# Kernel tuning notes

Measured on AMD Instinct MI355X. Metric: run time of the kernel, lower is better.

The kernel has to match this reference:

```python
import jax, jax.numpy as jnp
import numpy as np

B, N, DIM, K, H, R = 128, 196, 384, 16, 6, 4  # batch, tokens, channels, bases, heads, adapter ratio


def setup_inputs() -> dict:
    key = jax.random.key(0)
    ks = jax.random.split(key, 4)
    d_r = DIM // R
    return {
        "x": jax.random.normal(ks[0], (B, N, DIM), jnp.float32),
        "W1": jax.random.normal(ks[1], (DIM, d_r), jnp.float32) * 0.02,
        "b1": jnp.zeros((d_r,), jnp.float32),
        "W2": jax.random.normal(ks[2], (d_r, K * H), jnp.float32) * 0.02,
        "b2": jnp.zeros((K * H,), jnp.float32),
        "weight_bank": jax.random.normal(ks[3], (K, N, N), jnp.float32) * 0.02,
    }


def reference(x, W1, b1, W2, b2, weight_bank):
    Bsz, n, C = x.shape
    hdim = C // H
    # adapter MLP: Linear -> GELU(exact/erf, torch default) -> Linear
    hid = jax.nn.gelu(x @ W1 + b1, approximate=False)
    mix = (hid @ W2 + b2).reshape(Bsz, n, K, H)
    # mode='softmax': normalize mixing policy over the k bases
    mix = jax.nn.softmax(mix, axis=2)
    # dynamic per-sample token-mixing matrix [B, n, n, H]
    weight = jnp.einsum('bnkh,knm->bnmh', mix, weight_bank)
    # mix tokens: contract over source token index n
    xh = x.reshape(Bsz, n, H, hdim)
    out = jnp.einsum('bnhc,bnmh->bmhc', xh, weight).reshape(Bsz, n, C)
    return out
```

## Files before the change

kernel.cpp:

```cpp
#include <hip/hip_runtime.h>
#include <math.h>

#define BB  128
#define NN  196
#define CDIM 384
#define KK  16
#define HH  6
#define DR  96
#define HD  64
#define MP  208
#define NCHUNK 7
#define PLANE 6656

typedef __attribute__((ext_vector_type(8))) short bf16x8;
typedef __attribute__((ext_vector_type(4))) float f32x4;

__device__ __forceinline__ unsigned short f2bf(float f) {
    unsigned u = __float_as_uint(f);
    u += 0x7FFFu + ((u >> 16) & 1u);
    return (unsigned short)(u >> 16);
}
__device__ __forceinline__ unsigned pk2bf(float lo, float hi) {
    return (unsigned)f2bf(lo) | ((unsigned)f2bf(hi) << 16);
}

union AFrag { unsigned u[4]; bf16x8 f; };

__global__ __launch_bounds__(256) void prep_kernel(
    const float* __restrict__ W1, const float* __restrict__ W2,
    const float* __restrict__ wb,
    unsigned short* __restrict__ W1T, unsigned short* __restrict__ W2T,
    unsigned short* __restrict__ wbT)
{
    const int bid = blockIdx.x;
    const int t   = threadIdx.x;
    if (bid < DR) {
        const int c = bid;
        for (int k = t; k < CDIM; k += 256)
            W1T[(size_t)c * CDIM + k] = f2bf(W1[(size_t)k * DR + c]);
        if (t < DR)
            W2T[(size_t)c * DR + t] = f2bf(W2[(size_t)t * DR + c]);
    } else {
        const int n = bid - DR;
        const int m = t;
        if (m < MP) {
            unsigned o[8] = {0u, 0u, 0u, 0u, 0u, 0u, 0u, 0u};
            if (n < NN && m < NN) {
                #pragma unroll
                for (int j = 0; j < 8; ++j) {
                    const float a = wb[((size_t)(2 * j)     * NN + n) * NN + m];
                    const float c = wb[((size_t)(2 * j + 1) * NN + n) * NN + m];
                    o[j] = pk2bf(a, c);
                }
            }
            unsigned* dst = (unsigned*)(wbT + ((size_t)n * MP + m) * KK);
            *(uint4*)dst       = make_uint4(o[0], o[1], o[2], o[3]);
            *(uint4*)(dst + 4) = make_uint4(o[4], o[5], o[6], o[7]);
        }
    }
}

__global__ __launch_bounds__(256, 3) void mixa_kernel(
    const float* __restrict__ x,  const unsigned short* __restrict__ W1T,
    const float* __restrict__ b1, const unsigned short* __restrict__ W2T,
    const float* __restrict__ b2, const unsigned short* __restrict__ wbT,
    unsigned short* __restrict__ A)
{
    __shared__ unsigned short hidb[32][104];
    __shared__ unsigned short msc[32][96];

    const int t    = threadIdx.x;
    const int w    = t >> 6;
    const int wm   = w & 1;
    const int wc   = w >> 1;
    const int lane = t & 63;
    const int l15  = lane & 15;
    const int lq   = lane >> 4;
    const int b    = blockIdx.x & 127;
    const int nc   = blockIdx.x >> 7;
    const int n0   = nc * 32;

    f32x4 acc[3];
    #pragma unroll
    for (int ct = 0; ct < 3; ++ct) {
        const float bj = b1[wc * 48 + ct * 16 + l15];
        acc[ct] = (f32x4){bj, bj, bj, bj};
    }
    const int nrow = n0 + wm * 16 + l15;
    const bool rv  = (nrow < NN);
    const float* xrow = x + ((size_t)b * NN + nrow) * CDIM;
    float4 u = make_float4(0.f, 0.f, 0.f, 0.f);
    float4 v = make_float4(0.f, 0.f, 0.f, 0.f);
    if (rv) {
        u = *(const float4*)(xrow + 8 * lq);
        v = *(const float4*)(xrow + 8 * lq + 4);
    }
    for (int kc = 0; kc < CDIM; kc += 32) {
        float4 un = make_float4(0.f, 0.f, 0.f, 0.f);
        float4 vn = make_float4(0.f, 0.f, 0.f, 0.f);
        if (rv && kc + 32 < CDIM) {
            un = *(const float4*)(xrow + kc + 32 + 8 * lq);
            vn = *(const float4*)(xrow + kc + 32 + 8 * lq + 4);
        }
        __builtin_amdgcn_sched_barrier(0);
        AFrag af;
        af.u[0] = pk2bf(u.x, u.y); af.u[1] = pk2bf(u.z, u.w);
        af.u[2] = pk2bf(v.x, v.y); af.u[3] = pk2bf(v.z, v.w);
        #pragma unroll
        for (int ct = 0; ct < 3; ++ct) {
            const bf16x8 bf = *(const bf16x8*)(W1T + (size_t)(wc * 48 + ct * 16 + l15) * CDIM + kc + 8 * lq);
            acc[ct] = __builtin_amdgcn_mfma_f32_16x16x32_bf16(af.f, bf, acc[ct], 0, 0, 0);
        }
        __builtin_amdgcn_sched_barrier(0);
        u = un; v = vn;
    }
    #pragma unroll
    for (int ct = 0; ct < 3; ++ct)
        #pragma unroll
        for (int r = 0; r < 4; ++r) {
            const float vv = acc[ct][r];
            hidb[wm * 16 + lq * 4 + r][wc * 48 + ct * 16 + l15] =
                f2bf(0.5f * vv * (1.0f + erff(vv * 0.70710678118654752f)));
        }
    __syncthreads();

    f32x4 acc2[3];
    #pragma unroll
    for (int ct = 0; ct < 3; ++ct) {
        const float bj = b2[wc * 48 + ct * 16 + l15];
        acc2[ct] = (f32x4){bj, bj, bj, bj};
    }
    #pragma unroll
    for (int kc = 0; kc < DR; kc += 32) {
        const bf16x8 af = *(const bf16x8*)&hidb[wm * 16 + l15][kc + 8 * lq];
        #pragma unroll
        for (int ct = 0; ct < 3; ++ct) {
            const bf16x8 bf = *(const bf16x8*)(W2T + (size_t)(wc * 48 + ct * 16 + l15) * DR + kc + 8 * lq);
            acc2[ct] = __builtin_amdgcn_mfma_f32_16x16x32_bf16(af, bf, acc2[ct], 0, 0, 0);
        }
    }
    __syncthreads();

    #pragma unroll
    for (int ct = 0; ct < 3; ++ct)
        #pragma unroll
        for (int r = 0; r < 4; ++r)
            hidb[wm * 16 + lq * 4 + r][wc * 48 + ct * 16 + l15] = f2bf(acc2[ct][r]);
    __syncthreads();

    if (t < 192) {
        const int r = t / 6, h = t - r * 6;
        float lg[KK];
        float mx = -1e30f;
        #pragma unroll
        for (int k = 0; k < KK; ++k) {
            lg[k] = __uint_as_float((unsigned)hidb[r][6 * k + h] << 16);
            mx = fmaxf(mx, lg[k]);
        }
        float s = 0.f;
        #pragma unroll
        for (int k = 0; k < KK; ++k) { lg[k] = __expf(lg[k] - mx); s += lg[k]; }
        const float inv = 1.0f / s;
        unsigned o[8];
        #pragma unroll
        for (int jj = 0; jj < 8; ++jj)
            o[jj] = pk2bf(lg[2 * jj] * inv, lg[2 * jj + 1] * inv);
        unsigned* op = (unsigned*)&msc[r][16 * h];
        *(uint4*)op       = make_uint4(o[0], o[1], o[2], o[3]);
        *(uint4*)(op + 4) = make_uint4(o[4], o[5], o[6], o[7]);
    }
    __syncthreads();

    const bf16x8 z8 = {0, 0, 0, 0, 0, 0, 0, 0};
    const f32x4  cz = {0.f, 0.f, 0.f, 0.f};
    const size_t bc6 = ((size_t)b * NCHUNK + nc) * HH;
    const bool kv = (lq < 2);
    const bool hv = (l15 < HH);

    const unsigned short* wp0 = wbT + ((size_t)n0 * MP + l15) * KK + 8 * lq;

    bf16x8 ta[13], tb[13];
    {
        const unsigned short* wp = wp0 + (size_t)w * (MP * KK);
        #pragma unroll
        for (int mt = 0; mt < 13; ++mt)
            ta[mt] = *(const bf16x8*)(wp + mt * 256);
    }
    __builtin_amdgcn_sched_barrier(0);

    #pragma unroll
    for (int ii = 0; ii < 4; ++ii) {
        {
            const int nl = 8 * ii + w;
            {
                const unsigned short* wp = wp0 + (size_t)(nl + 4) * (MP * KK);
                #pragma unroll
                for (int mt = 0; mt < 13; ++mt)
                    tb[mt] = *(const bf16x8*)(wp + mt * 256);
            }
            __builtin_amdgcn_sched_barrier(0);
            const bf16x8 bmix = (hv && kv)
                ? *(const bf16x8*)&msc[nl][l15 * 16 + 8 * lq] : z8;
            unsigned short* p0 = A + (bc6 + l15) * PLANE + (size_t)nl * MP + lq * 4;
            #pragma unroll
            for (int mt = 0; mt < 13; ++mt) {
                const f32x4 c = __builtin_amdgcn_mfma_f32_16x16x32_bf16(ta[mt], bmix, cz, 0, 0, 0);
                if (hv) {
                    *(uint2*)(p0 + mt * 16) =
                        make_uint2(pk2bf(c[0], c[1]), pk2bf(c[2], c[3]));
                }
            }
            __builtin_amdgcn_sched_barrier(0);
        }
        {
            const int nl = 8 * ii + w + 4;
            if (ii < 3) {
                const unsigned short* wp = wp0 + (size_t)(nl + 4) * (MP * KK);
                #pragma unroll
                for (int mt = 0; mt < 13; ++mt)
                    ta[mt] = *(const bf16x8*)(wp + mt * 256);
            }
            __builtin_amdgcn_sched_barrier(0);
            const bf16x8 bmix = (hv && kv)
                ? *(const bf16x8*)&msc[nl][l15 * 16 + 8 * lq] : z8;
            unsigned short* p0 = A + (bc6 + l15) * PLANE + (size_t)nl * MP + lq * 4;
            #pragma unroll
            for (int mt = 0; mt < 13; ++mt) {
                const f32x4 c = __builtin_amdgcn_mfma_f32_16x16x32_bf16(tb[mt], bmix, cz, 0, 0, 0);
                if (hv) {
                    *(uint2*)(p0 + mt * 16) =
                        make_uint2(pk2bf(c[0], c[1]), pk2bf(c[2], c[3]));
                }
            }
            __builtin_amdgcn_sched_barrier(0);
        }
    }
}

__global__ __launch_bounds__(192, 3) void mix_gemm_kernel(
    const float* __restrict__ x, const unsigned short* __restrict__ Ab,
    float* __restrict__ out)
{
    __shared__ unsigned short xT[192][40];
    __shared__ unsigned short As[3][32][68];

    const int t    = threadIdx.x;
    const int bid  = blockIdx.x;
    const int b    = bid & 127;
    const int sub  = bid >> 7;
    const int q    = sub >> 1;
    const int hp   = sub & 1;
    const int m0   = q * 52;
    const int qvalid = (q == 3) ? 40 : 52;
    const int lw   = t >> 6;
    const int hbase = hp * 3;
    const int lane = t & 63;
    const int l15  = lane & 15;
    const int lq   = lane >> 4;
    const int c0   = hp * 192;

    const f32x4 cz = {0.f, 0.f, 0.f, 0.f};
    f32x4 acc[4][4];
    #pragma unroll
    for (int mt = 0; mt < 4; ++mt)
        #pragma unroll
        for (int ct = 0; ct < 4; ++ct) acc[mt][ct] = cz;

    unsigned long long av[8];

    {
        const size_t bc6 = (size_t)b * NCHUNK * HH + hbase;
        #pragma unroll
        for (int i = 0; i < 8; ++i) {
            const int P = t + 192 * i;
            const int row = P >> 4, p = P & 15;
            av[i] = *(const unsigned long long*)(
                Ab + (bc6 + (size_t)(row >> 5)) * PLANE + (size_t)(row & 31) * MP + m0 + 4 * p);
        }
    }

    for (int nc = 0; nc < NCHUNK; ++nc) {
        const int n0 = nc * 32;
        if (nc) __syncthreads();

        #pragma unroll
        for (int i = 0; i < 8; ++i) {
            const int P = t + 192 * i;
            const int row = P >> 4, p = P & 15;
            *(unsigned long long*)&As[row >> 5][row & 31][4 * p] = av[i];
        }

        #pragma unroll
        for (int it = 0; it < 4; ++it) {
            const int task = t + 192 * it;
            const int p  = task & 15;
            const int cq = task >> 4;
            const int n  = n0 + 2 * p;
            float4 va = make_float4(0.f, 0.f, 0.f, 0.f);
            float4 vb = make_float4(0.f, 0.f, 0.f, 0.f);
            if (n < NN)     va = *(const float4*)(x + ((size_t)b * NN + n) * CDIM + c0 + 4 * cq);
            if (n + 1 < NN) vb = *(const float4*)(x + ((size_t)b * NN + n + 1) * CDIM + c0 + 4 * cq);
            *(unsigned*)&xT[4 * cq + 0][2 * p] = pk2bf(va.x, vb.x);
            *(unsigned*)&xT[4 * cq + 1][2 * p] = pk2bf(va.y, vb.y);
            *(unsigned*)&xT[4 * cq + 2][2 * p] = pk2bf(va.z, vb.z);
            *(unsigned*)&xT[4 * cq + 3][2 * p] = pk2bf(va.w, vb.w);
        }
        __syncthreads();

        if (nc + 1 < NCHUNK) {
            const size_t bc6 = ((size_t)b * NCHUNK + nc + 1) * HH + hbase;
            #pragma unroll
            for (int i = 0; i < 8; ++i) {
                const int P = t + 192 * i;
                const int row = P >> 4, p = P & 15;
                av[i] = *(const unsigned long long*)(
                    Ab + (bc6 + (size_t)(row >> 5)) * PLANE + (size_t)(row & 31) * MP + m0 + 4 * p);
            }
        }
        __builtin_amdgcn_sched_barrier(0);

        bf16x8 afr[4], bfr[4];
        #pragma unroll
        for (int mt = 0; mt < 4; ++mt) {
            union { unsigned short s[8]; bf16x8 v; } u;
            #pragma unroll
            for (int j = 0; j < 8; ++j)
                u.s[j] = As[lw][8 * lq + j][mt * 16 + l15];
            afr[mt] = u.v;
        }
        #pragma unroll
        for (int ct = 0; ct < 4; ++ct)
            bfr[ct] = *(const bf16x8*)&xT[lw * 64 + ct * 16 + l15][8 * lq];
        #pragma unroll
        for (int mt = 0; mt < 4; ++mt)
            #pragma unroll
            for (int ct = 0; ct < 4; ++ct)
                acc[mt][ct] = __builtin_amdgcn_mfma_f32_16x16x32_bf16(
                    afr[mt], bfr[ct], acc[mt][ct], 0, 0, 0);
    }

    const int h = hbase + lw;
    #pragma unroll
    for (int mt = 0; mt < 4; ++mt) {
        #pragma unroll
        for (int r = 0; r < 4; ++r) {
            const int ms = mt * 16 + lq * 4 + r;
            if (ms < qvalid) {
                float* op = out + ((size_t)b * NN + m0 + ms) * CDIM + h * HD + l15;
                #pragma unroll
                for (int ct = 0; ct < 4; ++ct)
                    op[ct * 16] = acc[mt][ct][r];
            }
        }
    }
}

__global__ __launch_bounds__(128, 3) void adapter_kernel(
    const float* __restrict__ x,   const unsigned short* __restrict__ W1T,
    const float* __restrict__ b1,  const unsigned short* __restrict__ W2T,
    const float* __restrict__ b2,  unsigned short* __restrict__ mix_out)
{
    __shared__ unsigned short hidb[16][104];

    const int t    = threadIdx.x;
    const int wc   = t >> 6;
    const int lane = t & 63;
    const int l15  = lane & 15;
    const int lq   = lane >> 4;
    const int row0 = blockIdx.x * 16;

    f32x4 acc[3];
    #pragma unroll
    for (int ct = 0; ct < 3; ++ct) {
        const float bj = b1[wc * 48 + ct * 16 + l15];
        acc[ct] = (f32x4){bj, bj, bj, bj};
    }
    const float* xrow = x + (size_t)(row0 + l15) * CDIM;
    for (int kc = 0; kc < CDIM; kc += 32) {
        const float4 u = *(const float4*)(xrow + kc + 8 * lq);
        const float4 v = *(const float4*)(xrow + kc + 8 * lq + 4);
        AFrag af;
        af.u[0] = pk2bf(u.x, u.y); af.u[1] = pk2bf(u.z, u.w);
        af.u[2] = pk2bf(v.x, v.y); af.u[3] = pk2bf(v.z, v.w);
        #pragma unroll
        for (int ct = 0; ct < 3; ++ct) {
            const bf16x8 bf = *(const bf16x8*)(W1T + (size_t)(wc * 48 + ct * 16 + l15) * CDIM + kc + 8 * lq);
            acc[ct] = __builtin_amdgcn_mfma_f32_16x16x32_bf16(af.f, bf, acc[ct], 0, 0, 0);
        }
    }
    #pragma unroll
    for (int ct = 0; ct < 3; ++ct)
        #pragma unroll
        for (int r = 0; r < 4; ++r) {
            const float vv = acc[ct][r];
            hidb[lq * 4 + r][wc * 48 + ct * 16 + l15] =
                f2bf(0.5f * vv * (1.0f + erff(vv * 0.70710678118654752f)));
        }
    __syncthreads();

    f32x4 acc2[3];
    #pragma unroll
    for (int ct = 0; ct < 3; ++ct) {
        const float bj = b2[wc * 48 + ct * 16 + l15];
        acc2[ct] = (f32x4){bj, bj, bj, bj};
    }
    #pragma unroll
    for (int kc = 0; kc < DR; kc += 32) {
        const bf16x8 af = *(const bf16x8*)&hidb[l15][kc + 8 * lq];
        #pragma unroll
        for (int ct = 0; ct < 3; ++ct) {
            const bf16x8 bf = *(const bf16x8*)(W2T + (size_t)(wc * 48 + ct * 16 + l15) * DR + kc + 8 * lq);
            acc2[ct] = __builtin_amdgcn_mfma_f32_16x16x32_bf16(af, bf, acc2[ct], 0, 0, 0);
        }
    }
    __syncthreads();

    #pragma unroll
    for (int ct = 0; ct < 3; ++ct)
        #pragma unroll
        for (int r = 0; r < 4; ++r)
            hidb[lq * 4 + r][wc * 48 + ct * 16 + l15] = f2bf(acc2[ct][r]);
    __syncthreads();

    if (t < 96) {
        const int r = t / 6, h = t % 6;
        float lg[KK];
        float mx = -1e30f;
        #pragma unroll
        for (int k = 0; k < KK; ++k) {
            lg[k] = __uint_as_float((unsigned)hidb[r][6 * k + h] << 16);
            mx = fmaxf(mx, lg[k]);
        }
        float s = 0.f;
        #pragma unroll
        for (int k = 0; k < KK; ++k) { lg[k] = __expf(lg[k] - mx); s += lg[k]; }
        const float inv = 1.0f / s;
        unsigned o[8];
        #pragma unroll
        for (int jj = 0; jj < 8; ++jj)
            o[jj] = pk2bf(lg[2 * jj] * inv, lg[2 * jj + 1] * inv);
        unsigned* op = (unsigned*)(mix_out + ((size_t)(row0 + r) * HH + h) * KK);
        *(uint4*)op       = make_uint4(o[0], o[1], o[2], o[3]);
        *(uint4*)(op + 4) = make_uint4(o[4], o[5], o[6], o[7]);
    }
}

__global__ __launch_bounds__(192, 3) void mix_mfma_fb_kernel(
    const float* __restrict__ x,  const unsigned short* __restrict__ mixb,
    const unsigned short* __restrict__ wbT, float* __restrict__ out)
{
    __shared__ unsigned short xT[192][40];
    __shared__ unsigned short Asb[3][64][40];

    const int t    = threadIdx.x;
    const int bid  = blockIdx.x;
    const int b    = bid & 127;
    const int sub  = bid >> 7;
    const int q    = sub >> 1;
    const int hp   = sub & 1;
    const int m0   = q * 52;
    const int qvalid = (q == 3) ? 40 : 52;
    const int lw   = t >> 6;
    const int hbase = hp * 3;
    const int lane = t & 63;
    const int l15  = lane & 15;
    const int lq   = lane >> 4;
    const int c0   = hp * 192;

    const bf16x8 z8 = {0, 0, 0, 0, 0, 0, 0, 0};
    const f32x4  cz = {0.f, 0.f, 0.f, 0.f};

    f32x4 acc[4][4];
    #pragma unroll
    for (int mt = 0; mt < 4; ++mt)
        #pragma unroll
        for (int ct = 0; ct < 4; ++ct) acc[mt][ct] = cz;

    for (int nc = 0; nc < 7; ++nc) {
        const int n0 = nc * 32;
        __syncthreads();

        #pragma unroll
        for (int it = 0; it < 4; ++it) {
            const int task = t + 192 * it;
            const int p  = task & 15;
            const int cq = task >> 4;
            const int n  = n0 + 2 * p;
            float4 va = make_float4(0.f, 0.f, 0.f, 0.f);
            float4 vb = make_float4(0.f, 0.f, 0.f, 0.f);
            if (n < NN)     va = *(const float4*)(x + ((size_t)b * NN + n) * CDIM + c0 + 4 * cq);
            if (n + 1 < NN) vb = *(const float4*)(x + ((size_t)b * NN + n + 1) * CDIM + c0 + 4 * cq);
            *(unsigned*)&xT[4 * cq + 0][2 * p] = pk2bf(va.x, vb.x);
            *(unsigned*)&xT[4 * cq + 1][2 * p] = pk2bf(va.y, vb.y);
            *(unsigned*)&xT[4 * cq + 2][2 * p] = pk2bf(va.z, vb.z);
            *(unsigned*)&xT[4 * cq + 3][2 * p] = pk2bf(va.w, vb.w);
        }

        for (int nl = lw; nl < 32; nl += 3) {
            const int n = n0 + nl;
            if (n < NN) {
                bf16x8 af = z8;
                if (l15 < HH && lq < 2)
                    af = *(const bf16x8*)(mixb + (((size_t)b * NN + n) * HH + l15) * KK + 8 * lq);
                #pragma unroll
                for (int mt = 0; mt < 4; ++mt) {
                    const int m = m0 + mt * 16 + l15;
                    bf16x8 bf = z8;
                    if (lq < 2 && m < NN)
                        bf = *(const bf16x8*)(wbT + ((size_t)n * MP + m) * KK + 8 * lq);
                    const f32x4 c = __builtin_amdgcn_mfma_f32_16x16x32_bf16(af, bf, cz, 0, 0, 0);
                    #pragma unroll
                    for (int r = 0; r < 4; ++r) {
                        const int hh = lq * 4 + r;
                        if (hh >= hbase && hh < hbase + 3)
                            Asb[hh - hbase][mt * 16 + l15][nl] = f2bf(c[r]);
                    }
                }
            } else {
                #pragma unroll
                for (int mt = 0; mt < 4; ++mt)
                    #pragma unroll
                    for (int r = 0; r < 4; ++r) {
                        const int hh = lq * 4 + r;
                        if (hh >= hbase && hh < hbase + 3)
                            Asb[hh - hbase][mt * 16 + l15][nl] = 0;
                    }
            }
        }
        __syncthreads();

        bf16x8 afr[4], bfr[4];
        #pragma unroll
        for (int mt = 0; mt < 4; ++mt)
            afr[mt] = *(const bf16x8*)&Asb[lw][mt * 16 + l15][8 * lq];
        #pragma unroll
        for (int ct = 0; ct < 4; ++ct)
            bfr[ct] = *(const bf16x8*)&xT[lw * 64 + ct * 16 + l15][8 * lq];
        #pragma unroll
        for (int mt = 0; mt < 4; ++mt)
            #pragma unroll
            for (int ct = 0; ct < 4; ++ct)
                acc[mt][ct] = __builtin_amdgcn_mfma_f32_16x16x32_bf16(
                    afr[mt], bfr[ct], acc[mt][ct], 0, 0, 0);
    }

    const int h = hbase + lw;
    #pragma unroll
    for (int mt = 0; mt < 4; ++mt) {
        #pragma unroll
        for (int r = 0; r < 4; ++r) {
            const int ms = mt * 16 + lq * 4 + r;
            if (ms < qvalid) {
                float* op = out + ((size_t)b * NN + m0 + ms) * CDIM + h * HD + l15;
                #pragma unroll
                for (int ct = 0; ct < 4; ++ct)
                    op[ct * 16] = acc[mt][ct][r];
            }
        }
    }
}

extern "C" void kernel_launch(void* const* d_in, const int* in_sizes, int n_in,
                              void* d_out, int out_size, void* d_ws, size_t ws_size,
                              hipStream_t stream) {
    (void)in_sizes; (void)n_in; (void)out_size;
    const float* x  = (const float*)d_in[0];
    const float* W1 = (const float*)d_in[1];
    const float* b1 = (const float*)d_in[2];
    const float* W2 = (const float*)d_in[3];
    const float* b2 = (const float*)d_in[4];
    const float* wb = (const float*)d_in[5];
    float* out = (float*)d_out;

    const size_t W1T_OFF  = 0;
    const size_t W2T_OFF  = 73728;
    const size_t WBT_OFF  = 92160;
    const size_t A_OFF    = 1584128;
    const size_t NEED     = A_OFF + 71565312ull + 1024ull;

    unsigned short* w1t = (unsigned short*)((char*)d_ws + W1T_OFF);
    unsigned short* w2t = (unsigned short*)((char*)d_ws + W2T_OFF);
    unsigned short* wbt = (unsigned short*)((char*)d_ws + WBT_OFF);

    prep_kernel<<<DR + 224, 256, 0, stream>>>(W1, W2, wb, w1t, w2t, wbt);

    if (ws_size >= NEED) {
        unsigned short* Ab = (unsigned short*)((char*)d_ws + A_OFF);
        mixa_kernel<<<BB * NCHUNK, 256, 0, stream>>>(x, w1t, b1, w2t, b2, wbt, Ab);
        mix_gemm_kernel<<<8 * BB, 192, 0, stream>>>(x, Ab, out);
    } else {
        unsigned short* mixbuf = (unsigned short*)((char*)d_ws + A_OFF);
        adapter_kernel<<<(BB * NN) / 16, 128, 0, stream>>>(x, w1t, b1, w2t, b2, mixbuf);
        mix_mfma_fb_kernel<<<8 * BB, 192, 0, stream>>>(x, mixbuf, wbt, out);
    }
}
```

Measured before the change: 193.6 us.

## Split mixa_kernel A-formation across two blocks by m-tile halves

Doubles the mixa_kernel grid so each block forms only half of the m-tiles (7 or 6) of the per-sample mixing matrix. This halves the register arrays holding weight-bank fragments, which allows the launch bound to rise from 3 to 4 blocks per SM for better latency hiding. Several scheduling barriers are also removed, and the LDS mix load moves ahead of the prefetch. In exchange, the adapter MLP and softmax phase is now computed twice per (batch, chunk), duplicating that work.

```diff
diff --git a/kernel.cpp b/kernel.cpp
--- a/kernel.cpp
+++ b/kernel.cpp
@@ -60,7 +60,73 @@
     }
 }
 
-__global__ __launch_bounds__(256, 3) void mixa_kernel(
+template<int MT0, int NMT>
+__device__ __forceinline__ void aform_phase2(
+    const unsigned short* __restrict__ wbT, unsigned short* __restrict__ A,
+    const unsigned short (*msc)[96], int n0, size_t bc6,
+    int w, int l15, int lq)
+{
+    const bf16x8 z8 = {0, 0, 0, 0, 0, 0, 0, 0};
+    const f32x4  cz = {0.f, 0.f, 0.f, 0.f};
+    const bool kv = (lq < 2);
+    const bool hv = (l15 < HH);
+
+    const unsigned short* wp0 = wbT + ((size_t)n0 * MP + MT0 * 16 + l15) * KK + 8 * lq;
+
+    bf16x8 ta[NMT], tb[NMT];
+    {
+        const unsigned short* wp = wp0 + (size_t)w * (MP * KK);
+        #pragma unroll
+        for (int mt = 0; mt < NMT; ++mt)
+            ta[mt] = *(const bf16x8*)(wp + mt * 256);
+    }
+
+    #pragma unroll
+    for (int ii = 0; ii < 4; ++ii) {
+        {
+            const int nl = 8 * ii + w;
+            const bf16x8 bmix = (hv && kv)
+                ? *(const bf16x8*)&msc[nl][l15 * 16 + 8 * lq] : z8;
+            {
+                const unsigned short* wp = wp0 + (size_t)(nl + 4) * (MP * KK);
+                #pragma unroll
+                for (int mt = 0; mt < NMT; ++mt)
+                    tb[mt] = *(const bf16x8*)(wp + mt * 256);
+            }
+            __builtin_amdgcn_sched_barrier(0);
+            unsigned short* p0 = A + (bc6 + l15) * PLANE + (size_t)nl * MP + MT0 * 16 + lq * 4;
+            #pragma unroll
+            for (int mt = 0; mt < NMT; ++mt) {
+                const f32x4 c = __builtin_amdgcn_mfma_f32_16x16x32_bf16(ta[mt], bmix, cz, 0, 0, 0);
+                if (hv)
+                    *(uint2*)(p0 + mt * 16) =
+                        make_uint2(pk2bf(c[0], c[1]), pk2bf(c[2], c[3]));
+            }
+        }
+        {
+            const int nl = 8 * ii + w + 4;
+            const bf16x8 bmix = (hv && kv)
+                ? *(const bf16x8*)&msc[nl][l15 * 16 + 8 * lq] : z8;
+            if (ii < 3) {
+                const unsigned short* wp = wp0 + (size_t)(nl + 4) * (MP * KK);
+                #pragma unroll
+                for (int mt = 0; mt < NMT; ++mt)
+                    ta[mt] = *(const bf16x8*)(wp + mt * 256);
+            }
+            __builtin_amdgcn_sched_barrier(0);
+            unsigned short* p0 = A + (bc6 + l15) * PLANE + (size_t)nl * MP + MT0 * 16 + lq * 4;
+            #pragma unroll
+            for (int mt = 0; mt < NMT; ++mt) {
+                const f32x4 c = __builtin_amdgcn_mfma_f32_16x16x32_bf16(tb[mt], bmix, cz, 0, 0, 0);
+                if (hv)
+                    *(uint2*)(p0 + mt * 16) =
+                        make_uint2(pk2bf(c[0], c[1]), pk2bf(c[2], c[3]));
+            }
+        }
+    }
+}
+
+__global__ __launch_bounds__(256, 4) void mixa_kernel(
     const float* __restrict__ x,  const unsigned short* __restrict__ W1T,
     const float* __restrict__ b1, const unsigned short* __restrict__ W2T,
     const float* __restrict__ b2, const unsigned short* __restrict__ wbT,
@@ -77,7 +143,9 @@
     const int l15  = lane & 15;
     const int lq   = lane >> 4;
     const int b    = blockIdx.x & 127;
-    const int nc   = blockIdx.x >> 7;
+    const int sub  = blockIdx.x >> 7;
+    const int nc   = sub >> 1;
+    const int mh   = sub & 1;
     const int n0   = nc * 32;
 
     f32x4 acc[3];
@@ -102,7 +170,6 @@
             un = *(const float4*)(xrow + kc + 32 + 8 * lq);
             vn = *(const float4*)(xrow + kc + 32 + 8 * lq + 4);
         }
-        __builtin_amdgcn_sched_barrier(0);
         AFrag af;
         af.u[0] = pk2bf(u.x, u.y); af.u[1] = pk2bf(u.z, u.w);
         af.u[2] = pk2bf(v.x, v.y); af.u[3] = pk2bf(v.z, v.w);
@@ -111,7 +178,6 @@
             const bf16x8 bf = *(const bf16x8*)(W1T + (size_t)(wc * 48 + ct * 16 + l15) * CDIM + kc + 8 * lq);
             acc[ct] = __builtin_amdgcn_mfma_f32_16x16x32_bf16(af.f, bf, acc[ct], 0, 0, 0);
         }
-        __builtin_amdgcn_sched_barrier(0);
         u = un; v = vn;
     }
     #pragma unroll
@@ -171,70 +237,11 @@
     }
     __syncthreads();
 
-    const bf16x8 z8 = {0, 0, 0, 0, 0, 0, 0, 0};
-    const f32x4  cz = {0.f, 0.f, 0.f, 0.f};
     const size_t bc6 = ((size_t)b * NCHUNK + nc) * HH;
-    const bool kv = (lq < 2);
-    const bool hv = (l15 < HH);
-
-    const unsigned short* wp0 = wbT + ((size_t)n0 * MP + l15) * KK + 8 * lq;
-
-    bf16x8 ta[13], tb[13];
-    {
-        const unsigned short* wp = wp0 + (size_t)w * (MP * KK);
-        #pragma unroll
-        for (int mt = 0; mt < 13; ++mt)
-            ta[mt] = *(const bf16x8*)(wp + mt * 256);
-    }
-    __builtin_amdgcn_sched_barrier(0);
-
-    #pragma unroll
-    for (int ii = 0; ii < 4; ++ii) {
-        {
-            const int nl = 8 * ii + w;
-            {
-                const unsigned short* wp = wp0 + (size_t)(nl + 4) * (MP * KK);
-                #pragma unroll
-                for (int mt = 0; mt < 13; ++mt)
-                    tb[mt] = *(const bf16x8*)(wp + mt * 256);
-            }
-            __builtin_amdgcn_sched_barrier(0);
-            const bf16x8 bmix = (hv && kv)
-                ? *(const bf16x8*)&msc[nl][l15 * 16 + 8 * lq] : z8;
-            unsigned short* p0 = A + (bc6 + l15) * PLANE + (size_t)nl * MP + lq * 4;
-            #pragma unroll
-            for (int mt = 0; mt < 13; ++mt) {
-                const f32x4 c = __builtin_amdgcn_mfma_f32_16x16x32_bf16(ta[mt], bmix, cz, 0, 0, 0);
-                if (hv) {
-                    *(uint2*)(p0 + mt * 16) =
-                        make_uint2(pk2bf(c[0], c[1]), pk2bf(c[2], c[3]));
-                }
-            }
-            __builtin_amdgcn_sched_barrier(0);
-        }
-        {
-            const int nl = 8 * ii + w + 4;
-            if (ii < 3) {
-                const unsigned short* wp = wp0 + (size_t)(nl + 4) * (MP * KK);
-                #pragma unroll
-                for (int mt = 0; mt < 13; ++mt)
-                    ta[mt] = *(const bf16x8*)(wp + mt * 256);
-            }
-            __builtin_amdgcn_sched_barrier(0);
-            const bf16x8 bmix = (hv && kv)
-                ? *(const bf16x8*)&msc[nl][l15 * 16 + 8 * lq] : z8;
-            unsigned short* p0 = A + (bc6 + l15) * PLANE + (size_t)nl * MP + lq * 4;
-            #pragma unroll
-            for (int mt = 0; mt < 13; ++mt) {
-                const f32x4 c = __builtin_amdgcn_mfma_f32_16x16x32_bf16(tb[mt], bmix, cz, 0, 0, 0);
-                if (hv) {
-                    *(uint2*)(p0 + mt * 16) =
-                        make_uint2(pk2bf(c[0], c[1]), pk2bf(c[2], c[3]));
-                }
-            }
-            __builtin_amdgcn_sched_barrier(0);
-        }
-    }
+    if (mh == 0)
+        aform_phase2<0, 7>(wbT, A, msc, n0, bc6, w, l15, lq);
+    else
+        aform_phase2<7, 6>(wbT, A, msc, n0, bc6, w, l15, lq);
 }
 
 __global__ __launch_bounds__(192, 3) void mix_gemm_kernel(
@@ -586,7 +593,7 @@
 
     if (ws_size >= NEED) {
         unsigned short* Ab = (unsigned short*)((char*)d_ws + A_OFF);
-        mixa_kernel<<<BB * NCHUNK, 256, 0, stream>>>(x, w1t, b1, w2t, b2, wbt, Ab);
+        mixa_kernel<<<BB * NCHUNK * 2, 256, 0, stream>>>(x, w1t, b1, w2t, b2, wbt, Ab);
         mix_gemm_kernel<<<8 * BB, 192, 0, stream>>>(x, Ab, out);
     } else {
         unsigned short* mixbuf = (unsigned short*)((char*)d_ws + A_OFF);
```

New measurement: 210.2 us. 1.09x slower.
